# Kernel optimization log

Hardware: AMD Instinct MI355X
Metric: run time of the kernel (lower is better)

The kernel has to match this reference:

```python
import jax, jax.numpy as jnp
import numpy as np

N_NODES = 50000


def setup_inputs() -> dict:
    key = jax.random.key(0)
    k1, k2, k3, k4, k5, k6 = jax.random.split(key, 6)
    c_in, c_out = 64, 64
    n_edges = 800000
    G = jax.random.normal(k1, (N_NODES, c_in), dtype=jnp.float32)
    RSC = jax.random.normal(k2, (N_NODES, c_in), dtype=jnp.float32)
    src = jax.random.randint(k3, (n_edges,), 0, N_NODES, dtype=jnp.int64)
    dst = jax.random.randint(k4, (n_edges,), 0, N_NODES, dtype=jnp.int64)
    W = jax.random.normal(k5, (c_out, c_in), dtype=jnp.float32) / np.sqrt(c_in)
    b = jax.random.normal(k6, (c_out,), dtype=jnp.float32) * 0.01
    return {"G": G, "RSC": RSC, "src": src, "dst": dst, "W": W, "b": b}


def reference(G, RSC, src, dst, W, b):
    # Per-edge relative feature: src node 'G' feature minus dst node 'RSC' feature
    rel = G[src] - RSC[dst]                          # [E, c_in]
    # Linear + ReLU (edge MLP)
    enc = jax.nn.relu(rel @ W.T + b)                 # [E, c_out]
    # Per-dst-node reductions over variable-size mailboxes
    max_agg = jax.ops.segment_max(enc, dst, num_segments=N_NODES)  # -inf for empty
    sum_agg = jax.ops.segment_sum(enc, dst, num_segments=N_NODES)
    cnt = jax.ops.segment_sum(jnp.ones_like(dst, dtype=enc.dtype), dst,
                              num_segments=N_NODES)               # [N]
    has_mail = (cnt > 0)[:, None]
    avg_agg = sum_agg / jnp.maximum(cnt, 1.0)[:, None]
    max_agg = jnp.where(has_mail, max_agg, 0.0)      # nodes w/o edges -> 0
    # concat(max, avg) as in reduce()
    return jnp.concatenate([max_agg, avg_agg], axis=-1)  # [N, 2*c_out]
```

## Files before the change

kernel.cpp:

```cpp
#include <hip/hip_runtime.h>
#include <hip/hip_bf16.h>

#define NCH 64
#define SPAN 64
#define HIST_BLOCKS 256
#define HIST_THREADS 1024
#define NBIN 256
#define NGEMM 256
#define FUSE_THREADS 512
#define SORT_CAP 3072

__global__ void detect_init_kernel(const unsigned short* __restrict__ gp, int n16,
                                   const unsigned* __restrict__ ip, int niw,
                                   unsigned* __restrict__ flags,
                                   unsigned* __restrict__ gcnt, int nb) {
    if (blockIdx.x == 0) {
        __shared__ unsigned se, so;
        if (threadIdx.x == 0) { se = 0u; so = 0u; }
        __syncthreads();
        unsigned le = 0u, lo = 0u;
        for (int i = threadIdx.x; i < n16; i += blockDim.x) {
            unsigned ex = (unsigned)((gp[i] >> 7) & 0xFFu);
            if (ex >= 0xC0u) le++;
        }
        for (int i = threadIdx.x; i < niw; i += blockDim.x) {
            if ((i & 1) && ip[i] != 0u) lo++;
        }
        atomicAdd(&se, le);
        atomicAdd(&so, lo);
        __syncthreads();
        if (threadIdx.x == 0) {
            flags[0] = (se > 50u) ? 1u : 0u;
            flags[1] = (so < 50u) ? 1u : 0u;
        }
    } else {
        const int stride = (gridDim.x - 1) * blockDim.x;
        for (int i = (blockIdx.x - 1) * blockDim.x + threadIdx.x; i < nb; i += stride)
            gcnt[i] = 0u;
    }
}

__global__ void bucket_hist_kernel(const void* __restrict__ dstp,
                                   unsigned* __restrict__ gcnt,
                                   const unsigned* __restrict__ flags,
                                   int n_edges, int nb) {
    extern __shared__ unsigned lcnt[];
    for (int i = threadIdx.x; i < nb; i += blockDim.x) lcnt[i] = 0u;
    __syncthreads();
    const unsigned i64 = flags[1];
    const int stride = gridDim.x * blockDim.x;
    for (int e = blockIdx.x * blockDim.x + threadIdx.x; e < n_edges; e += stride) {
        int d = i64 ? (int)((const long long*)dstp)[e] : ((const int*)dstp)[e];
        atomicAdd(&lcnt[d >> 6], 1u);
    }
    __syncthreads();
    for (int i = threadIdx.x; i < nb; i += blockDim.x)
        if (lcnt[i]) atomicAdd(&gcnt[i], lcnt[i]);
}

__global__ void bucket_scan_kernel(const unsigned* __restrict__ gcnt,
                                   unsigned* __restrict__ boffs,
                                   unsigned* __restrict__ cursor, int nb) {
    __shared__ unsigned s[1024];
    const int t = threadIdx.x;
    const int L = (nb + 1023) / 1024;
    unsigned local = 0u;
    for (int i = 0; i < L; ++i) {
        int idx = t * L + i;
        if (idx < nb) local += gcnt[idx];
    }
    s[t] = local;
    __syncthreads();
    for (int off = 1; off < 1024; off <<= 1) {
        unsigned v = (t >= off) ? s[t - off] : 0u;
        __syncthreads();
        s[t] += v;
        __syncthreads();
    }
    unsigned run = s[t] - local;
    for (int i = 0; i < L; ++i) {
        int idx = t * L + i;
        if (idx < nb) { boffs[idx] = run; cursor[idx] = run; run += gcnt[idx]; }
    }
}

__global__ __launch_bounds__(FUSE_THREADS, 4)
void binning_gemm_kernel(const void* __restrict__ srcp, const void* __restrict__ dstp,
                         unsigned* __restrict__ cursor, unsigned* __restrict__ binned,
                         const unsigned* __restrict__ flags, int n_edges, int nb,
                         int depth,
                         const void* __restrict__ Gp, const void* __restrict__ Rp,
                         const void* __restrict__ Wp, const void* __restrict__ bp,
                         void* __restrict__ PQ, int n_nodes) {
    extern __shared__ unsigned lds[];
    if (blockIdx.x < NBIN) {
        unsigned* lcnt = lds;
        unsigned* stage = lds + nb;
        for (int i = threadIdx.x; i < nb; i += blockDim.x) lcnt[i] = 0u;
        __syncthreads();
        const unsigned i64 = flags[1];
        const int chunk = (n_edges + NBIN - 1) / NBIN;
        const int e0 = blockIdx.x * chunk;
        const int e1 = min(e0 + chunk, n_edges);
        for (int e = e0 + threadIdx.x; e < e1; e += blockDim.x) {
            int s, d;
            if (i64) {
                s = (int)((const long long*)srcp)[e];
                d = (int)((const long long*)dstp)[e];
            } else {
                s = ((const int*)srcp)[e];
                d = ((const int*)dstp)[e];
            }
            const int bkt = d >> 6;
            const unsigned pk = ((unsigned)(d & 63) << 26) | (unsigned)s;
            unsigned pos = atomicAdd(&lcnt[bkt], 1u);
            if ((int)pos < depth) {
                stage[bkt * depth + (int)pos] = pk;
            } else {
                unsigned g = atomicAdd(&cursor[bkt], 1u);
                binned[g] = pk;
            }
        }
        __syncthreads();
        for (int bkt = threadIdx.x; bkt < nb; bkt += blockDim.x) {
            int k = min((int)lcnt[bkt], depth);
            if (k > 0) {
                unsigned base = atomicAdd(&cursor[bkt], (unsigned)k);
                for (int i = 0; i < k; ++i) binned[base + i] = stage[bkt * depth + i];
            }
        }
    } else {
        const unsigned f32 = flags[0];
        const int lane = threadIdx.x & 63;
        const int waveInBlk = threadIdx.x >> 6;
        const int wavesPerBlk = blockDim.x >> 6;
        const int gwave = (blockIdx.x - NBIN) * wavesPerBlk + waveInBlk;
        const int nwaves = NGEMM * wavesPerBlk;
        const int n_rows = 2 * n_nodes;
        const int ngroups = (n_rows + 3) / 4;

        float* ldsb = (float*)lds;
        float* slot = &ldsb[waveInBlk * 4 * NCH];

        float w[NCH];
        float bias;
        if (f32) {
            const float* Wf = (const float*)Wp;
            #pragma unroll
            for (int k = 0; k < NCH; ++k) w[k] = Wf[lane * NCH + k];
            bias = ((const float*)bp)[lane];
        } else {
            const __hip_bfloat16* Wh = (const __hip_bfloat16*)Wp;
            #pragma unroll
            for (int k = 0; k < NCH; ++k) w[k] = __bfloat162float(Wh[lane * NCH + k]);
            bias = __bfloat162float(((const __hip_bfloat16*)bp)[lane]);
        }

        const int niter = (ngroups + nwaves - 1) / nwaves;
        for (int it = 0; it < niter; ++it) {
            const int grp = gwave + it * nwaves;
            const bool gvalid = (grp < ngroups);
            const int m0 = grp * 4;
            if (gvalid) {
                const int myrow = m0 + (lane >> 4);
                const int col = (lane & 15) * 4;
                float x0 = 0.f, x1 = 0.f, x2 = 0.f, x3 = 0.f;
                if (myrow < n_rows) {
                    const bool isQ = (myrow >= n_nodes);
                    const int r = isQ ? (myrow - n_nodes) : myrow;
                    const void* inp = isQ ? Rp : Gp;
                    if (f32) {
                        float4 v = *(const float4*)((const float*)inp +
                                                    (size_t)r * NCH + col);
                        x0 = v.x; x1 = v.y; x2 = v.z; x3 = v.w;
                    } else {
                        ushort4 v = *(const ushort4*)((const unsigned short*)inp +
                                                      (size_t)r * NCH + col);
                        x0 = __bfloat162float(*(__hip_bfloat16*)&v.x);
                        x1 = __bfloat162float(*(__hip_bfloat16*)&v.y);
                        x2 = __bfloat162float(*(__hip_bfloat16*)&v.z);
                        x3 = __bfloat162float(*(__hip_bfloat16*)&v.w);
                    }
                }
                const int sb = (lane >> 4) * NCH + col;
                slot[sb + 0] = x0; slot[sb + 1] = x1;
                slot[sb + 2] = x2; slot[sb + 3] = x3;
            }
            __syncthreads();
            if (gvalid) {
                #pragma unroll
                for (int rr = 0; rr < 4; ++rr) {
                    const int m = m0 + rr;
                    if (m < n_rows) {
                        float a0 = 0.f, a1 = 0.f, a2 = 0.f, a3 = 0.f;
                        const float4* r4 = (const float4*)(slot + rr * NCH);
                        #pragma unroll
                        for (int q = 0; q < 16; ++q) {
                            float4 rv = r4[q];
                            a0 = fmaf(rv.x, w[4 * q + 0], a0);
                            a1 = fmaf(rv.y, w[4 * q + 1], a1);
                            a2 = fmaf(rv.z, w[4 * q + 2], a2);
                            a3 = fmaf(rv.w, w[4 * q + 3], a3);
                        }
                        float acc = (a0 + a1) + (a2 + a3);
                        if (m >= n_nodes) acc -= bias;
                        if (f32) ((float*)PQ)[(size_t)m * NCH + lane] = acc;
                        else ((__hip_bfloat16*)PQ)[(size_t)m * NCH + lane] =
                                 __float2bfloat16(acc);
                    }
                }
            }
            __syncthreads();
        }
    }
}

__global__ __launch_bounds__(256)
void bucket_sort_kernel(const unsigned* __restrict__ binned,
                        const unsigned* __restrict__ boffs,
                        const unsigned* __restrict__ gcnt,
                        unsigned* __restrict__ sorted_src,
                        unsigned* __restrict__ offs,
                        int n_nodes, int n_edges, int nb) {
    __shared__ unsigned dcnt[SPAN];
    __shared__ unsigned doff[SPAN];
    __shared__ unsigned cur[SPAN];
    __shared__ unsigned stage[SORT_CAP];
    const int b = blockIdx.x;
    const int tid = threadIdx.x;
    const int estart = (int)boffs[b];
    const int count = (int)gcnt[b];

    if (tid < SPAN) dcnt[tid] = 0u;
    __syncthreads();

    for (int i = tid; i < count; i += 256) {
        const unsigned pk = binned[estart + i];
        atomicAdd(&dcnt[pk >> 26], 1u);
        if (i < SORT_CAP) stage[i] = pk;
    }
    __syncthreads();

    if (tid == 0) {
        unsigned run = 0u;
        #pragma unroll
        for (int i = 0; i < SPAN; ++i) { doff[i] = run; cur[i] = run; run += dcnt[i]; }
    }
    __syncthreads();

    if (tid < SPAN) {
        const int n = b * SPAN + tid;
        if (n < n_nodes) offs[n] = (unsigned)estart + doff[tid];
    }
    if (b == nb - 1 && tid == 0) offs[n_nodes] = (unsigned)n_edges;

    const int lim = (count < SORT_CAP) ? count : SORT_CAP;
    for (int i = tid; i < lim; i += 256) {
        const unsigned pk = stage[i];
        const unsigned pos = atomicAdd(&cur[pk >> 26], 1u);
        sorted_src[estart + pos] = pk & 0x03FFFFFFu;
    }
    for (int i = SORT_CAP + tid; i < count; i += 256) {
        const unsigned pk = binned[estart + i];
        const unsigned pos = atomicAdd(&cur[pk >> 26], 1u);
        sorted_src[estart + pos] = pk & 0x03FFFFFFu;
    }
}

__global__ void node_kernel(const void* __restrict__ PQ,
                            const unsigned* __restrict__ sorted_src,
                            const unsigned* __restrict__ offs,
                            const unsigned* __restrict__ flags,
                            void* __restrict__ outp, int n_nodes) {
    const unsigned f32 = flags[0];
    const int lane = threadIdx.x & 63;
    const int gwave = (blockIdx.x * blockDim.x + threadIdx.x) >> 6;
    const int nwaves = (gridDim.x * blockDim.x) >> 6;
    const float* Pf = (const float*)PQ;
    const unsigned short* Ph = (const unsigned short*)PQ;

    for (int n = gwave; n < n_nodes; n += nwaves) {
        float q;
        if (f32) q = Pf[(size_t)(n_nodes + n) * NCH + lane];
        else {
            unsigned short h = Ph[(size_t)(n_nodes + n) * NCH + lane];
            q = __bfloat162float(*(__hip_bfloat16*)&h);
        }
        const int start = (int)offs[n];
        const int end = (int)offs[n + 1];
        float vmax = 0.0f, vsum = 0.0f;
        int j = start;
        for (; j + 4 <= end; j += 4) {
            const int s0 = (int)sorted_src[j];
            const int s1 = (int)sorted_src[j + 1];
            const int s2 = (int)sorted_src[j + 2];
            const int s3 = (int)sorted_src[j + 3];
            float p0, p1, p2, p3;
            if (f32) {
                p0 = Pf[(size_t)s0 * NCH + lane];
                p1 = Pf[(size_t)s1 * NCH + lane];
                p2 = Pf[(size_t)s2 * NCH + lane];
                p3 = Pf[(size_t)s3 * NCH + lane];
            } else {
                unsigned short h0 = Ph[(size_t)s0 * NCH + lane];
                unsigned short h1 = Ph[(size_t)s1 * NCH + lane];
                unsigned short h2 = Ph[(size_t)s2 * NCH + lane];
                unsigned short h3 = Ph[(size_t)s3 * NCH + lane];
                p0 = __bfloat162float(*(__hip_bfloat16*)&h0);
                p1 = __bfloat162float(*(__hip_bfloat16*)&h1);
                p2 = __bfloat162float(*(__hip_bfloat16*)&h2);
                p3 = __bfloat162float(*(__hip_bfloat16*)&h3);
            }
            const float v0 = fmaxf(p0 - q, 0.0f);
            const float v1 = fmaxf(p1 - q, 0.0f);
            const float v2 = fmaxf(p2 - q, 0.0f);
            const float v3 = fmaxf(p3 - q, 0.0f);
            vmax = fmaxf(fmaxf(vmax, v0), fmaxf(v1, fmaxf(v2, v3)));
            vsum += (v0 + v1) + (v2 + v3);
        }
        for (; j < end; ++j) {
            const int s = (int)sorted_src[j];
            float p;
            if (f32) p = Pf[(size_t)s * NCH + lane];
            else {
                unsigned short h = Ph[(size_t)s * NCH + lane];
                p = __bfloat162float(*(__hip_bfloat16*)&h);
            }
            const float v = fmaxf(p - q, 0.0f);
            vmax = fmaxf(vmax, v);
            vsum += v;
        }
        const int deg = end - start;
        const float avg = vsum / (float)(deg > 0 ? deg : 1);
        if (f32) {
            float* out = (float*)outp;
            out[(size_t)n * 2 * NCH + lane] = vmax;
            out[(size_t)n * 2 * NCH + NCH + lane] = avg;
        } else {
            __hip_bfloat16* out = (__hip_bfloat16*)outp;
            out[(size_t)n * 2 * NCH + lane] = __float2bfloat16(vmax);
            out[(size_t)n * 2 * NCH + NCH + lane] = __float2bfloat16(avg);
        }
    }
}

extern "C" void kernel_launch(void* const* d_in, const int* in_sizes, int n_in,
                              void* d_out, int out_size, void* d_ws, size_t ws_size,
                              hipStream_t stream) {
    const void* G = d_in[0];
    const void* RSC = d_in[1];
    const void* src = d_in[2];
    const void* dst = d_in[3];
    const void* W = d_in[4];
    const void* b = d_in[5];

    const int n_nodes = in_sizes[0] / NCH;
    const int n_edges = in_sizes[2];
    const int nb = (n_nodes + SPAN - 1) / SPAN;

    char* ws = (char*)d_ws;
    unsigned* flags = (unsigned*)ws;
    size_t off = 256;
    unsigned* binned = (unsigned*)(ws + off);
    off += (((size_t)n_edges * 4 + 255) / 256) * 256;
    unsigned* sorted_src = (unsigned*)(ws + off);
    off += (((size_t)n_edges * 4 + 255) / 256) * 256;
    unsigned* offs = (unsigned*)(ws + off);
    off += (((size_t)(n_nodes + 1) * 4 + 255) / 256) * 256;
    unsigned* boffs = (unsigned*)(ws + off);
    off += (((size_t)nb * 4 + 255) / 256) * 256;
    unsigned* cursor = (unsigned*)(ws + off);
    off += (((size_t)nb * 4 + 255) / 256) * 256;
    unsigned* gcnt = (unsigned*)(ws + off);
    off += (((size_t)nb * 4 + 255) / 256) * 256;
    void* PQ = (void*)(ws + off);

    const int n_g_probe = (in_sizes[0] < 8192) ? in_sizes[0] : 8192;
    const int n_idx_probe = (n_edges < 8192) ? n_edges : 8192;

    detect_init_kernel<<<64, 256, 0, stream>>>((const unsigned short*)G, n_g_probe,
                                               (const unsigned*)src, n_idx_probe,
                                               flags, gcnt, nb);

    bucket_hist_kernel<<<HIST_BLOCKS, HIST_THREADS, (size_t)nb * 4, stream>>>(
        dst, gcnt, flags, n_edges, nb);

    bucket_scan_kernel<<<1, 1024, 0, stream>>>(gcnt, boffs, cursor, nb);

    int depth = 16384 / nb - 1;
    if (depth > 19) depth = 19;
    if (depth < 4) depth = 4;
    size_t bin_lds = (size_t)nb * (depth + 1) * 4;
    const size_t gemm_lds = (size_t)(FUSE_THREADS / 64) * 4 * NCH * 4;
    if (bin_lds < gemm_lds) bin_lds = gemm_lds;

    binning_gemm_kernel<<<NBIN + NGEMM, FUSE_THREADS, bin_lds, stream>>>(
        src, dst, cursor, binned, flags, n_edges, nb, depth,
        G, RSC, W, b, PQ, n_nodes);

    bucket_sort_kernel<<<nb, 256, 0, stream>>>(binned, boffs, gcnt, sorted_src,
                                               offs, n_nodes, n_edges, nb);

    node_kernel<<<2048, 256, 0, stream>>>(PQ, sorted_src, offs, flags, d_out, n_nodes);
}
```

Before: 194.0 us.

## Split node gather into half-waves with float2 loads; raise fused-kernel occupancy

Each 64-lane wave in node_kernel now processes two edges at once: each half-wave gathers one edge's 64 channels with 2-element vector loads, and the halves are merged with a cross-half shuffle at the end. This doubles the bytes per load instruction and halves the loop trip count, aiming to increase memory-level parallelism in the latency-bound gather. The fused binning/GEMM kernel also gets three times as many GEMM blocks, a higher launch-bounds occupancy target, and a smaller per-bin LDS staging depth so more blocks fit per CU. The trade-off is more register pressure and less staging per bin, which may add extra global writes.

```diff
diff --git a/kernel.cpp b/kernel.cpp
--- a/kernel.cpp
+++ b/kernel.cpp
@@ -6,7 +6,7 @@
 #define HIST_BLOCKS 256
 #define HIST_THREADS 1024
 #define NBIN 256
-#define NGEMM 256
+#define NGEMM 768
 #define FUSE_THREADS 512
 #define SORT_CAP 3072
 
@@ -84,7 +84,7 @@
     }
 }
 
-__global__ __launch_bounds__(FUSE_THREADS, 4)
+__global__ __launch_bounds__(FUSE_THREADS, 8)
 void binning_gemm_kernel(const void* __restrict__ srcp, const void* __restrict__ dstp,
                          unsigned* __restrict__ cursor, unsigned* __restrict__ binned,
                          const unsigned* __restrict__ flags, int n_edges, int nb,
@@ -267,79 +267,116 @@
     }
 }
 
-__global__ void node_kernel(const void* __restrict__ PQ,
-                            const unsigned* __restrict__ sorted_src,
-                            const unsigned* __restrict__ offs,
-                            const unsigned* __restrict__ flags,
-                            void* __restrict__ outp, int n_nodes) {
+__global__ __launch_bounds__(256)
+void node_kernel(const void* __restrict__ PQ,
+                 const unsigned* __restrict__ sorted_src,
+                 const unsigned* __restrict__ offs,
+                 const unsigned* __restrict__ flags,
+                 void* __restrict__ outp, int n_nodes) {
     const unsigned f32 = flags[0];
     const int lane = threadIdx.x & 63;
+    const int h = lane >> 5;
+    const int c2 = lane & 31;
     const int gwave = (blockIdx.x * blockDim.x + threadIdx.x) >> 6;
     const int nwaves = (gridDim.x * blockDim.x) >> 6;
     const float* Pf = (const float*)PQ;
     const unsigned short* Ph = (const unsigned short*)PQ;
 
     for (int n = gwave; n < n_nodes; n += nwaves) {
-        float q;
-        if (f32) q = Pf[(size_t)(n_nodes + n) * NCH + lane];
-        else {
-            unsigned short h = Ph[(size_t)(n_nodes + n) * NCH + lane];
-            q = __bfloat162float(*(__hip_bfloat16*)&h);
+        float q0, q1;
+        if (f32) {
+            float2 qq = *(const float2*)&Pf[(size_t)(n_nodes + n) * NCH + 2 * c2];
+            q0 = qq.x; q1 = qq.y;
+        } else {
+            ushort2 qq = *(const ushort2*)&Ph[(size_t)(n_nodes + n) * NCH + 2 * c2];
+            q0 = __bfloat162float(*(__hip_bfloat16*)&qq.x);
+            q1 = __bfloat162float(*(__hip_bfloat16*)&qq.y);
         }
         const int start = (int)offs[n];
         const int end = (int)offs[n + 1];
-        float vmax = 0.0f, vsum = 0.0f;
+        float m0 = 0.f, m1 = 0.f, s0 = 0.f, s1 = 0.f;
         int j = start;
-        for (; j + 4 <= end; j += 4) {
-            const int s0 = (int)sorted_src[j];
-            const int s1 = (int)sorted_src[j + 1];
-            const int s2 = (int)sorted_src[j + 2];
-            const int s3 = (int)sorted_src[j + 3];
-            float p0, p1, p2, p3;
+        for (; j + 8 <= end; j += 8) {
+            const int i0 = j + h;
+            const int e0 = (int)sorted_src[i0];
+            const int e1 = (int)sorted_src[i0 + 2];
+            const int e2 = (int)sorted_src[i0 + 4];
+            const int e3 = (int)sorted_src[i0 + 6];
+            float p00, p01, p10, p11, p20, p21, p30, p31;
             if (f32) {
-                p0 = Pf[(size_t)s0 * NCH + lane];
-                p1 = Pf[(size_t)s1 * NCH + lane];
-                p2 = Pf[(size_t)s2 * NCH + lane];
-                p3 = Pf[(size_t)s3 * NCH + lane];
+                float2 v0 = *(const float2*)&Pf[(size_t)e0 * NCH + 2 * c2];
+                float2 v1 = *(const float2*)&Pf[(size_t)e1 * NCH + 2 * c2];
+                float2 v2 = *(const float2*)&Pf[(size_t)e2 * NCH + 2 * c2];
+                float2 v3 = *(const float2*)&Pf[(size_t)e3 * NCH + 2 * c2];
+                p00 = v0.x; p01 = v0.y; p10 = v1.x; p11 = v1.y;
+                p20 = v2.x; p21 = v2.y; p30 = v3.x; p31 = v3.y;
             } else {
-                unsigned short h0 = Ph[(size_t)s0 * NCH + lane];
-                unsigned short h1 = Ph[(size_t)s1 * NCH + lane];
-                unsigned short h2 = Ph[(size_t)s2 * NCH + lane];
-                unsigned short h3 = Ph[(size_t)s3 * NCH + lane];
-                p0 = __bfloat162float(*(__hip_bfloat16*)&h0);
-                p1 = __bfloat162float(*(__hip_bfloat16*)&h1);
-                p2 = __bfloat162float(*(__hip_bfloat16*)&h2);
-                p3 = __bfloat162float(*(__hip_bfloat16*)&h3);
-            }
-            const float v0 = fmaxf(p0 - q, 0.0f);
-            const float v1 = fmaxf(p1 - q, 0.0f);
-            const float v2 = fmaxf(p2 - q, 0.0f);
-            const float v3 = fmaxf(p3 - q, 0.0f);
-            vmax = fmaxf(fmaxf(vmax, v0), fmaxf(v1, fmaxf(v2, v3)));
-            vsum += (v0 + v1) + (v2 + v3);
-        }
-        for (; j < end; ++j) {
-            const int s = (int)sorted_src[j];
-            float p;
-            if (f32) p = Pf[(size_t)s * NCH + lane];
-            else {
-                unsigned short h = Ph[(size_t)s * NCH + lane];
-                p = __bfloat162float(*(__hip_bfloat16*)&h);
-            }
-            const float v = fmaxf(p - q, 0.0f);
-            vmax = fmaxf(vmax, v);
-            vsum += v;
-        }
+                ushort2 u0 = *(const ushort2*)&Ph[(size_t)e0 * NCH + 2 * c2];
+                ushort2 u1 = *(const ushort2*)&Ph[(size_t)e1 * NCH + 2 * c2];
+                ushort2 u2 = *(const ushort2*)&Ph[(size_t)e2 * NCH + 2 * c2];
+                ushort2 u3 = *(const ushort2*)&Ph[(size_t)e3 * NCH + 2 * c2];
+                p00 = __bfloat162float(*(__hip_bfloat16*)&u0.x);
+                p01 = __bfloat162float(*(__hip_bfloat16*)&u0.y);
+                p10 = __bfloat162float(*(__hip_bfloat16*)&u1.x);
+                p11 = __bfloat162float(*(__hip_bfloat16*)&u1.y);
+                p20 = __bfloat162float(*(__hip_bfloat16*)&u2.x);
+                p21 = __bfloat162float(*(__hip_bfloat16*)&u2.y);
+                p30 = __bfloat162float(*(__hip_bfloat16*)&u3.x);
+                p31 = __bfloat162float(*(__hip_bfloat16*)&u3.y);
+            }
+            const float v00 = fmaxf(p00 - q0, 0.f), v01 = fmaxf(p01 - q1, 0.f);
+            const float v10 = fmaxf(p10 - q0, 0.f), v11 = fmaxf(p11 - q1, 0.f);
+            const float v20 = fmaxf(p20 - q0, 0.f), v21 = fmaxf(p21 - q1, 0.f);
+            const float v30 = fmaxf(p30 - q0, 0.f), v31 = fmaxf(p31 - q1, 0.f);
+            m0 = fmaxf(fmaxf(m0, v00), fmaxf(v10, fmaxf(v20, v30)));
+            m1 = fmaxf(fmaxf(m1, v01), fmaxf(v11, fmaxf(v21, v31)));
+            s0 += (v00 + v10) + (v20 + v30);
+            s1 += (v01 + v11) + (v21 + v31);
+        }
+        #pragma unroll
+        for (int u = 0; u < 4; ++u) {
+            const int idx = j + 2 * u + h;
+            if (idx < end) {
+                const int e = (int)sorted_src[idx];
+                float p0, p1;
+                if (f32) {
+                    float2 v = *(const float2*)&Pf[(size_t)e * NCH + 2 * c2];
+                    p0 = v.x; p1 = v.y;
+                } else {
+                    ushort2 uu = *(const ushort2*)&Ph[(size_t)e * NCH + 2 * c2];
+                    p0 = __bfloat162float(*(__hip_bfloat16*)&uu.x);
+                    p1 = __bfloat162float(*(__hip_bfloat16*)&uu.y);
+                }
+                const float v0 = fmaxf(p0 - q0, 0.f);
+                const float v1 = fmaxf(p1 - q1, 0.f);
+                m0 = fmaxf(m0, v0); m1 = fmaxf(m1, v1);
+                s0 += v0; s1 += v1;
+            }
+        }
+        m0 = fmaxf(m0, __shfl_xor(m0, 32));
+        m1 = fmaxf(m1, __shfl_xor(m1, 32));
+        s0 = s0 + __shfl_xor(s0, 32);
+        s1 = s1 + __shfl_xor(s1, 32);
         const int deg = end - start;
-        const float avg = vsum / (float)(deg > 0 ? deg : 1);
-        if (f32) {
-            float* out = (float*)outp;
-            out[(size_t)n * 2 * NCH + lane] = vmax;
-            out[(size_t)n * 2 * NCH + NCH + lane] = avg;
-        } else {
-            __hip_bfloat16* out = (__hip_bfloat16*)outp;
-            out[(size_t)n * 2 * NCH + lane] = __float2bfloat16(vmax);
-            out[(size_t)n * 2 * NCH + NCH + lane] = __float2bfloat16(avg);
+        const float inv = 1.0f / (float)(deg > 0 ? deg : 1);
+        const float a0 = s0 * inv, a1 = s1 * inv;
+        if (h == 0) {
+            if (f32) {
+                float* out = (float*)outp;
+                *(float2*)&out[(size_t)n * 2 * NCH + 2 * c2] = make_float2(m0, m1);
+                *(float2*)&out[(size_t)n * 2 * NCH + NCH + 2 * c2] = make_float2(a0, a1);
+            } else {
+                unsigned short* out = (unsigned short*)outp;
+                __hip_bfloat16 hm0 = __float2bfloat16(m0);
+                __hip_bfloat16 hm1 = __float2bfloat16(m1);
+                __hip_bfloat16 ha0 = __float2bfloat16(a0);
+                __hip_bfloat16 ha1 = __float2bfloat16(a1);
+                ushort2 sm, sa;
+                sm.x = *(unsigned short*)&hm0; sm.y = *(unsigned short*)&hm1;
+                sa.x = *(unsigned short*)&ha0; sa.y = *(unsigned short*)&ha1;
+                *(ushort2*)&out[(size_t)n * 2 * NCH + 2 * c2] = sm;
+                *(ushort2*)&out[(size_t)n * 2 * NCH + NCH + 2 * c2] = sa;
+            }
         }
     }
 }
@@ -387,7 +424,7 @@
 
     bucket_scan_kernel<<<1, 1024, 0, stream>>>(gcnt, boffs, cursor, nb);
 
-    int depth = 16384 / nb - 1;
+    int depth = 9728 / nb - 1;
     if (depth > 19) depth = 19;
     if (depth < 4) depth = 4;
     size_t bin_lds = (size_t)nb * (depth + 1) * 4;
```

Result: slower. 278.9 us (+43.7%).

## Fuse bucket sort into node aggregation kernel using LDS-resident sorted edges

Applied to the files above, without the earlier changes.

Merges the per-bucket counting sort and the per-node gather/reduce into one kernel. Each block sorts its bucket's packed edges in shared memory and then aggregates its 64 nodes directly, so the sorted_src and offs global arrays and one launch go away. Overflow edges beyond the LDS cap are handled by a slow per-node rescan of the bucket. It also adds more GEMM blocks to the fused binning/GEMM kernel and lowers the binning LDS depth, which trades per-block LDS for occupancy. The node grid drops to one block per bucket (about 782 blocks of 8 waves), so there is less latency hiding than the old 2048-block grid-stride launch.

```diff
diff --git a/kernel.cpp b/kernel.cpp
--- a/kernel.cpp
+++ b/kernel.cpp
@@ -6,9 +6,9 @@
 #define HIST_BLOCKS 256
 #define HIST_THREADS 1024
 #define NBIN 256
-#define NGEMM 256
+#define NGEMM 768
 #define FUSE_THREADS 512
-#define SORT_CAP 3072
+#define NB_CAP 1536
 
 __global__ void detect_init_kernel(const unsigned short* __restrict__ gp, int n16,
                                    const unsigned* __restrict__ ip, int niw,
@@ -215,97 +215,85 @@
     }
 }
 
-__global__ __launch_bounds__(256)
-void bucket_sort_kernel(const unsigned* __restrict__ binned,
+__global__ __launch_bounds__(512)
+void bucket_node_kernel(const unsigned* __restrict__ binned,
                         const unsigned* __restrict__ boffs,
                         const unsigned* __restrict__ gcnt,
-                        unsigned* __restrict__ sorted_src,
-                        unsigned* __restrict__ offs,
-                        int n_nodes, int n_edges, int nb) {
-    __shared__ unsigned dcnt[SPAN];
-    __shared__ unsigned doff[SPAN];
+                        const void* __restrict__ PQ,
+                        const unsigned* __restrict__ flags,
+                        void* __restrict__ outp, int n_nodes) {
+    __shared__ unsigned scnt[SPAN];
+    __shared__ unsigned soff[SPAN];
     __shared__ unsigned cur[SPAN];
-    __shared__ unsigned stage[SORT_CAP];
+    __shared__ unsigned dext[SPAN];
+    __shared__ unsigned stage[NB_CAP];
+    __shared__ unsigned sorted[NB_CAP];
+
     const int b = blockIdx.x;
     const int tid = threadIdx.x;
     const int estart = (int)boffs[b];
     const int count = (int)gcnt[b];
-
-    if (tid < SPAN) dcnt[tid] = 0u;
-    __syncthreads();
-
-    for (int i = tid; i < count; i += 256) {
+    const int lim = (count < NB_CAP) ? count : NB_CAP;
+
+    if (tid < SPAN) { scnt[tid] = 0u; dext[tid] = 0u; }
+    __syncthreads();
+
+    for (int i = tid; i < count; i += 512) {
         const unsigned pk = binned[estart + i];
-        atomicAdd(&dcnt[pk >> 26], 1u);
-        if (i < SORT_CAP) stage[i] = pk;
+        if (i < NB_CAP) { stage[i] = pk; atomicAdd(&scnt[pk >> 26], 1u); }
+        else atomicAdd(&dext[pk >> 26], 1u);
     }
     __syncthreads();
 
     if (tid == 0) {
         unsigned run = 0u;
         #pragma unroll
-        for (int i = 0; i < SPAN; ++i) { doff[i] = run; cur[i] = run; run += dcnt[i]; }
-    }
-    __syncthreads();
-
-    if (tid < SPAN) {
-        const int n = b * SPAN + tid;
-        if (n < n_nodes) offs[n] = (unsigned)estart + doff[tid];
-    }
-    if (b == nb - 1 && tid == 0) offs[n_nodes] = (unsigned)n_edges;
-
-    const int lim = (count < SORT_CAP) ? count : SORT_CAP;
-    for (int i = tid; i < lim; i += 256) {
+        for (int i = 0; i < SPAN; ++i) { soff[i] = run; cur[i] = run; run += scnt[i]; }
+    }
+    __syncthreads();
+
+    for (int i = tid; i < lim; i += 512) {
         const unsigned pk = stage[i];
         const unsigned pos = atomicAdd(&cur[pk >> 26], 1u);
-        sorted_src[estart + pos] = pk & 0x03FFFFFFu;
-    }
-    for (int i = SORT_CAP + tid; i < count; i += 256) {
-        const unsigned pk = binned[estart + i];
-        const unsigned pos = atomicAdd(&cur[pk >> 26], 1u);
-        sorted_src[estart + pos] = pk & 0x03FFFFFFu;
-    }
-}
-
-__global__ void node_kernel(const void* __restrict__ PQ,
-                            const unsigned* __restrict__ sorted_src,
-                            const unsigned* __restrict__ offs,
-                            const unsigned* __restrict__ flags,
-                            void* __restrict__ outp, int n_nodes) {
+        sorted[pos] = pk & 0x03FFFFFFu;
+    }
+    __syncthreads();
+
     const unsigned f32 = flags[0];
-    const int lane = threadIdx.x & 63;
-    const int gwave = (blockIdx.x * blockDim.x + threadIdx.x) >> 6;
-    const int nwaves = (gridDim.x * blockDim.x) >> 6;
+    const int lane = tid & 63;
+    const int wid = tid >> 6;
     const float* Pf = (const float*)PQ;
     const unsigned short* Ph = (const unsigned short*)PQ;
 
-    for (int n = gwave; n < n_nodes; n += nwaves) {
+    for (int nn = wid; nn < SPAN; nn += 8) {
+        const int n = b * SPAN + nn;
+        if (n >= n_nodes) break;
         float q;
         if (f32) q = Pf[(size_t)(n_nodes + n) * NCH + lane];
         else {
             unsigned short h = Ph[(size_t)(n_nodes + n) * NCH + lane];
             q = __bfloat162float(*(__hip_bfloat16*)&h);
         }
-        const int start = (int)offs[n];
-        const int end = (int)offs[n + 1];
+        const int s0i = (int)soff[nn];
+        const int scn = (int)scnt[nn];
         float vmax = 0.0f, vsum = 0.0f;
-        int j = start;
-        for (; j + 4 <= end; j += 4) {
-            const int s0 = (int)sorted_src[j];
-            const int s1 = (int)sorted_src[j + 1];
-            const int s2 = (int)sorted_src[j + 2];
-            const int s3 = (int)sorted_src[j + 3];
+        int j = 0;
+        for (; j + 4 <= scn; j += 4) {
+            const int e0 = (int)sorted[s0i + j];
+            const int e1 = (int)sorted[s0i + j + 1];
+            const int e2 = (int)sorted[s0i + j + 2];
+            const int e3 = (int)sorted[s0i + j + 3];
             float p0, p1, p2, p3;
             if (f32) {
-                p0 = Pf[(size_t)s0 * NCH + lane];
-                p1 = Pf[(size_t)s1 * NCH + lane];
-                p2 = Pf[(size_t)s2 * NCH + lane];
-                p3 = Pf[(size_t)s3 * NCH + lane];
+                p0 = Pf[(size_t)e0 * NCH + lane];
+                p1 = Pf[(size_t)e1 * NCH + lane];
+                p2 = Pf[(size_t)e2 * NCH + lane];
+                p3 = Pf[(size_t)e3 * NCH + lane];
             } else {
-                unsigned short h0 = Ph[(size_t)s0 * NCH + lane];
-                unsigned short h1 = Ph[(size_t)s1 * NCH + lane];
-                unsigned short h2 = Ph[(size_t)s2 * NCH + lane];
-                unsigned short h3 = Ph[(size_t)s3 * NCH + lane];
+                unsigned short h0 = Ph[(size_t)e0 * NCH + lane];
+                unsigned short h1 = Ph[(size_t)e1 * NCH + lane];
+                unsigned short h2 = Ph[(size_t)e2 * NCH + lane];
+                unsigned short h3 = Ph[(size_t)e3 * NCH + lane];
                 p0 = __bfloat162float(*(__hip_bfloat16*)&h0);
                 p1 = __bfloat162float(*(__hip_bfloat16*)&h1);
                 p2 = __bfloat162float(*(__hip_bfloat16*)&h2);
@@ -318,19 +306,34 @@
             vmax = fmaxf(fmaxf(vmax, v0), fmaxf(v1, fmaxf(v2, v3)));
             vsum += (v0 + v1) + (v2 + v3);
         }
-        for (; j < end; ++j) {
-            const int s = (int)sorted_src[j];
+        for (; j < scn; ++j) {
+            const int e = (int)sorted[s0i + j];
             float p;
-            if (f32) p = Pf[(size_t)s * NCH + lane];
+            if (f32) p = Pf[(size_t)e * NCH + lane];
             else {
-                unsigned short h = Ph[(size_t)s * NCH + lane];
+                unsigned short h = Ph[(size_t)e * NCH + lane];
                 p = __bfloat162float(*(__hip_bfloat16*)&h);
             }
             const float v = fmaxf(p - q, 0.0f);
             vmax = fmaxf(vmax, v);
             vsum += v;
         }
-        const int deg = end - start;
+        for (int i = NB_CAP; i < count; ++i) {
+            const unsigned pk = binned[estart + i];
+            if ((int)(pk >> 26) == nn) {
+                const int e = (int)(pk & 0x03FFFFFFu);
+                float p;
+                if (f32) p = Pf[(size_t)e * NCH + lane];
+                else {
+                    unsigned short h = Ph[(size_t)e * NCH + lane];
+                    p = __bfloat162float(*(__hip_bfloat16*)&h);
+                }
+                const float v = fmaxf(p - q, 0.0f);
+                vmax = fmaxf(vmax, v);
+                vsum += v;
+            }
+        }
+        const int deg = scn + (int)dext[nn];
         const float avg = vsum / (float)(deg > 0 ? deg : 1);
         if (f32) {
             float* out = (float*)outp;
@@ -363,10 +366,6 @@
     size_t off = 256;
     unsigned* binned = (unsigned*)(ws + off);
     off += (((size_t)n_edges * 4 + 255) / 256) * 256;
-    unsigned* sorted_src = (unsigned*)(ws + off);
-    off += (((size_t)n_edges * 4 + 255) / 256) * 256;
-    unsigned* offs = (unsigned*)(ws + off);
-    off += (((size_t)(n_nodes + 1) * 4 + 255) / 256) * 256;
     unsigned* boffs = (unsigned*)(ws + off);
     off += (((size_t)nb * 4 + 255) / 256) * 256;
     unsigned* cursor = (unsigned*)(ws + off);
@@ -387,7 +386,7 @@
 
     bucket_scan_kernel<<<1, 1024, 0, stream>>>(gcnt, boffs, cursor, nb);
 
-    int depth = 16384 / nb - 1;
+    int depth = 9728 / nb - 1;
     if (depth > 19) depth = 19;
     if (depth < 4) depth = 4;
     size_t bin_lds = (size_t)nb * (depth + 1) * 4;
@@ -398,8 +397,6 @@
         src, dst, cursor, binned, flags, n_edges, nb, depth,
         G, RSC, W, b, PQ, n_nodes);
 
-    bucket_sort_kernel<<<nb, 256, 0, stream>>>(binned, boffs, gcnt, sorted_src,
-                                               offs, n_nodes, n_edges, nb);
-
-    node_kernel<<<2048, 256, 0, stream>>>(PQ, sorted_src, offs, flags, d_out, n_nodes);
-}
+    bucket_node_kernel<<<nb, 512, 0, stream>>>(binned, boffs, gcnt, PQ, flags,
+                                               d_out, n_nodes);
+}
```

Result: faster. 184.3 us (-5.0%).
